# Optimization experiments

Hardware: AMD Instinct MI355X
Metric: run time of the kernel (lower is better)

## Reference

```python
import jax, jax.numpy as jnp
import numpy as np

N = 4096
IN_F = 256
OUT_F = 64
K = 4
ALPHA = 0.2  # LeakyReLU negative slope
NEG_INF = -9e15


def setup_inputs() -> dict:
    key = jax.random.key(0)
    k_h, k_w, k_a, k_e, k_m = jax.random.split(key, 5)
    h = jax.random.normal(k_h, (N, IN_F), dtype=jnp.float32)
    # xavier_uniform with gain=1.414
    def xavier(k, shape, gain=1.414):
        fan_in, fan_out = shape[0], shape[1]
        limit = gain * np.sqrt(6.0 / (fan_in + fan_out))
        return jax.random.uniform(k, shape, jnp.float32, -limit, limit)
    W = xavier(k_w, (IN_F, OUT_F))
    a = xavier(k_a, (2 * OUT_F, 1))
    vals = jax.random.uniform(k_e, (K, N, N), dtype=jnp.float32)
    mask = jax.random.uniform(k_m, (K, N, N), dtype=jnp.float32) < 0.05
    edge_attr = jnp.where(mask, vals, 0.0)
    return {"h": h, "edge_attr": edge_attr, "W": W, "a": a}


def reference(h, edge_attr, W, a):
    # h: [N, IN_F], edge_attr: [K, N, N], W: [IN_F, OUT_F], a: [2*OUT_F, 1]
    Wh = h @ W                                   # [N, OUT_F]
    Wh1 = Wh @ a[:OUT_F, :]                      # [N, 1]
    Wh2 = Wh @ a[OUT_F:, :]                      # [N, 1]
    e = jax.nn.leaky_relu(Wh1 + Wh2.T, negative_slope=ALPHA)  # [N, N]
    e = e[None, :, :] * edge_attr                # [K, N, N]
    e = jnp.where(edge_attr > 0, e, NEG_INF)
    att = jax.nn.softmax(e, axis=1)              # softmax over dim=1, as in torch
    # dropout is identity in eval mode
    # batched replacement for the per-channel python loop of matmuls
    hp = jnp.einsum('kij,jf->kif', att, Wh)      # [K, N, OUT_F]
    out = jnp.transpose(hp, (1, 0, 2)).reshape(N, K * OUT_F)  # concat dim=1
    return jax.nn.elu(out), att
```

## Files before the change

### kernel.cpp

```cpp
#include <hip/hip_runtime.h>

#define NN 4096
#define IN_F 256
#define OUT_F 64
#define K_CH 4
#define ALPHA 0.2f
#define JP 8
#define JCOLS 512
#define ROWS1 16
#define IC1 256

typedef __bf16 bf16;
typedef __attribute__((ext_vector_type(8))) __bf16 bf16x8;
typedef __attribute__((ext_vector_type(4))) float f32x4;

__global__ __launch_bounds__(256) void k0_wh(const float* __restrict__ h,
                                             const float* __restrict__ W,
                                             const float* __restrict__ a,
                                             float* __restrict__ Wh,
                                             float* __restrict__ Wh1,
                                             float* __restrict__ Wh2) {
    int tid = threadIdx.x;
    int wave = tid >> 6, lane = tid & 63;
    int i = blockIdx.x * 4 + wave;
    const float* hrow = h + (size_t)i * IN_F;
    float acc = 0.f;
    #pragma unroll 8
    for (int c = 0; c < IN_F; ++c)
        acc += hrow[c] * W[c * OUT_F + lane];
    Wh[(size_t)i * OUT_F + lane] = acc;
    float v1 = acc * a[lane];
    float v2 = acc * a[OUT_F + lane];
    #pragma unroll
    for (int o = 32; o > 0; o >>= 1) {
        v1 += __shfl_xor(v1, o, 64);
        v2 += __shfl_xor(v2, o, 64);
    }
    if (lane == 0) { Wh1[i] = v1; Wh2[i] = v2; }
}

__global__ __launch_bounds__(256) void k0_transpose(const float* __restrict__ Wh,
                                                    bf16* __restrict__ WhT) {
    __shared__ float lds[OUT_F * 65];
    int tid = threadIdx.x;
    int i0 = blockIdx.x * 64;
    int f = tid & 63;
    int r0 = tid >> 6;
    #pragma unroll
    for (int s = 0; s < 16; ++s) {
        int r = r0 * 16 + s;
        lds[f * 65 + r] = Wh[(size_t)(i0 + r) * OUT_F + f];
    }
    __syncthreads();
    int f2 = tid >> 2;
    int c0 = (tid & 3) * 16;
    #pragma unroll
    for (int s = 0; s < 16; ++s) {
        int c = c0 + s;
        WhT[(size_t)f2 * NN + i0 + c] = (bf16)lds[f2 * 65 + c];
    }
}

__global__ __launch_bounds__(256) void k1_colsum(const float* __restrict__ edge,
                                                 const float* __restrict__ Wh1,
                                                 const float* __restrict__ Wh2,
                                                 bf16* __restrict__ p_buf,
                                                 float* __restrict__ partial) {
    int tid = threadIdx.x;
    int kch = blockIdx.z;
    int j0 = blockIdx.y * 2048 + tid * 8;
    int ic = blockIdx.x;
    int ibase = ic * ROWS1;
    float w2[8];
    {
        f32x4 t0 = *(const f32x4*)&Wh2[j0];
        f32x4 t1 = *(const f32x4*)&Wh2[j0 + 4];
        #pragma unroll
        for (int c = 0; c < 4; ++c) { w2[c] = t0[c]; w2[c + 4] = t1[c]; }
    }
    float s[8] = {0.f, 0.f, 0.f, 0.f, 0.f, 0.f, 0.f, 0.f};
    const float* base = edge + ((size_t)kch * NN + ibase) * NN + j0;
    bf16* pbase = p_buf + ((size_t)kch * NN + ibase) * NN + j0;
    f32x4 r0[4], r1[4];
    #pragma unroll
    for (int t = 0; t < 4; ++t) {
        r0[t] = *(const f32x4*)(base + (size_t)t * NN);
        r1[t] = *(const f32x4*)(base + (size_t)t * NN + 4);
    }
    #pragma unroll 4
    for (int ii = 0; ii < ROWS1; ++ii) {
        int cur = ii & 3;
        f32x4 e0 = r0[cur], e1 = r1[cur];
        int ip = (ii + 4 < ROWS1) ? ii + 4 : ii;
        r0[cur] = *(const f32x4*)(base + (size_t)ip * NN);
        r1[cur] = *(const f32x4*)(base + (size_t)ip * NN + 4);
        float wh1 = Wh1[ibase + ii];
        bf16x8 pv;
        #pragma unroll
        for (int c = 0; c < 8; ++c) {
            float ef = c < 4 ? e0[c] : e1[c - 4];
            float xv = wh1 + w2[c];
            float lk = xv > 0.f ? xv : ALPHA * xv;
            float val = ef > 0.f ? __expf(lk * ef) : 0.f;
            bf16 vb = (bf16)val;
            pv[c] = vb;
            s[c] += (float)vb;
        }
        *(bf16x8*)(pbase + (size_t)ii * NN) = pv;
    }
    float* pr = partial + ((size_t)kch * IC1 + ic) * NN + j0;
    f32x4 o0, o1;
    #pragma unroll
    for (int c = 0; c < 4; ++c) { o0[c] = s[c]; o1[c] = s[c + 4]; }
    *(f32x4*)pr = o0;
    *(f32x4*)(pr + 4) = o1;
}

__global__ __launch_bounds__(256) void k1_reduce(const float* __restrict__ partial,
                                                 float* __restrict__ s_inv) {
    __shared__ float red[256];
    int tid = threadIdx.x;
    int kch = blockIdx.y;
    int jl = tid & 63, g = tid >> 6;
    int j = blockIdx.x * 64 + jl;
    const float* pb = partial + (size_t)kch * IC1 * NN;
    float s = 0.f;
    #pragma unroll 8
    for (int t = 0; t < IC1 / 4; ++t)
        s += pb[(size_t)(g * (IC1 / 4) + t) * NN + j];
    red[tid] = s;
    __syncthreads();
    if (tid < 64) {
        float tot = red[tid] + red[tid + 64] + red[tid + 128] + red[tid + 192];
        s_inv[kch * NN + j] = tot > 0.f ? 1.f / tot : 0.f;
    }
}

__global__ __launch_bounds__(256) void k2_fused(const bf16* __restrict__ p_buf,
                                                const float* __restrict__ s_inv,
                                                const bf16* __restrict__ WhT,
                                                float* __restrict__ att_out,
                                                float* __restrict__ hp) {
    __shared__ float lds_inv[JCOLS];
    int tid = threadIdx.x;
    int itile = blockIdx.x;
    int z = blockIdx.y;
    int kch = z >> 3, jp = z & 7;
    int jbase0 = jp * JCOLS;
    {
        int t2 = tid * 2;
        lds_inv[t2]     = s_inv[kch * NN + jbase0 + t2];
        lds_inv[t2 + 1] = s_inv[kch * NN + jbase0 + t2 + 1];
    }
    __syncthreads();
    int wave = tid >> 6, lane = tid & 63;
    int n16 = lane & 15, quad = lane >> 4;
    int i_row = itile * 64 + wave * 16 + n16;
    const size_t ebase = ((size_t)kch * NN + i_row) * NN + jbase0 + quad * 8;
    const bf16* pptr = p_buf + ebase;
    float* aptr = att_out + ebase;
    const bf16* wbase = WhT + (size_t)n16 * NN + jbase0 + quad * 8;
    f32x4 acc[4] = {};
    bf16x8 pf[4];
    #pragma unroll
    for (int t = 0; t < 4; ++t)
        pf[t] = *(const bf16x8*)(pptr + t * 32);
    #pragma unroll 4
    for (int s = 0; s < JCOLS / 32; ++s) {
        int cur = s & 3;
        bf16x8 pv = pf[cur];
        int sp = (s + 4 < JCOLS / 32) ? s + 4 : s;
        pf[cur] = *(const bf16x8*)(pptr + sp * 32);
        int jl = s * 32 + quad * 8;
        f32x4 iv0 = *(const f32x4*)&lds_inv[jl];
        f32x4 iv1 = *(const f32x4*)&lds_inv[jl + 4];
        bf16x8 afrag;
        f32x4 av0, av1;
        #pragma unroll
        for (int c = 0; c < 8; ++c) {
            float isc = c < 4 ? iv0[c] : iv1[c - 4];
            float attv = (float)pv[c] * isc;
            afrag[c] = (bf16)attv;
            if (c < 4) av0[c] = attv; else av1[c - 4] = attv;
        }
        __builtin_nontemporal_store(av0, (f32x4*)(aptr + s * 32));
        __builtin_nontemporal_store(av1, (f32x4*)(aptr + s * 32 + 4));
        #pragma unroll
        for (int ft = 0; ft < 4; ++ft) {
            bf16x8 bfrag = *(const bf16x8*)(wbase + (size_t)ft * 16 * NN + s * 32);
            acc[ft] = __builtin_amdgcn_mfma_f32_16x16x32_bf16(afrag, bfrag, acc[ft], 0, 0, 0);
        }
    }
    #pragma unroll
    for (int ft = 0; ft < 4; ++ft) {
        #pragma unroll
        for (int r = 0; r < 4; ++r) {
            int row_l = quad * 4 + r;
            int i_g = itile * 64 + wave * 16 + row_l;
            size_t idx = ((size_t)z * NN + i_g) * OUT_F + ft * 16 + n16;
            hp[idx] = acc[ft][r];
        }
    }
}

__global__ __launch_bounds__(256) void k3_combine(const float* __restrict__ hp,
                                                  float* __restrict__ out) {
    int g = blockIdx.x * 256 + threadIdx.x;
    int i = g >> 8;
    int rem = g & 255;
    int kch = rem >> 6;
    int f = rem & 63;
    float s = 0.f;
    #pragma unroll
    for (int z = 0; z < JP; ++z)
        s += hp[(((size_t)(kch * JP + z)) * NN + i) * OUT_F + f];
    out[g] = s > 0.f ? s : __expf(s) - 1.f;
}

extern "C" void kernel_launch(void* const* d_in, const int* in_sizes, int n_in,
                              void* d_out, int out_size, void* d_ws, size_t ws_size,
                              hipStream_t stream) {
    (void)out_size; (void)ws_size;
    const float *h = nullptr, *edge = nullptr, *W = nullptr, *a = nullptr;
    for (int i = 0; i < n_in; ++i) {
        int sz = in_sizes[i];
        if (sz == NN * IN_F)               h    = (const float*)d_in[i];
        else if (sz == K_CH * NN * NN)     edge = (const float*)d_in[i];
        else if (sz == IN_F * OUT_F)       W    = (const float*)d_in[i];
        else if (sz == 2 * OUT_F)          a    = (const float*)d_in[i];
    }

    char* ws = (char*)d_ws;
    size_t off = 0;
    float* Wh      = (float*)(ws + off); off += (size_t)NN * OUT_F * 4;
    float* Wh1     = (float*)(ws + off); off += NN * 4;
    float* Wh2     = (float*)(ws + off); off += NN * 4;
    float* s_inv   = (float*)(ws + off); off += (size_t)K_CH * NN * 4;
    bf16*  WhT     = (bf16*) (ws + off); off += (size_t)OUT_F * NN * 2;
    float* partial = (float*)(ws + off); off += (size_t)K_CH * IC1 * NN * 4;
    float* hp      = (float*)(ws + off); off += (size_t)K_CH * JP * NN * OUT_F * 4;
    bf16*  p_buf   = (bf16*) (ws + off); off += (size_t)K_CH * NN * NN * 2;

    float* out_h   = (float*)d_out;
    float* att_out = out_h + (size_t)NN * (K_CH * OUT_F);

    k0_wh<<<dim3(NN / 4), 256, 0, stream>>>(h, W, a, Wh, Wh1, Wh2);
    k0_transpose<<<dim3(NN / 64), 256, 0, stream>>>(Wh, WhT);
    k1_colsum<<<dim3(IC1, 2, K_CH), 256, 0, stream>>>(edge, Wh1, Wh2, p_buf, partial);
    k1_reduce<<<dim3(NN / 64, K_CH), 256, 0, stream>>>(partial, s_inv);
    k2_fused<<<dim3(64, K_CH * JP), 256, 0, stream>>>(p_buf, s_inv, WhT, att_out, hp);
    k3_combine<<<dim3((NN * K_CH * OUT_F) / 256), 256, 0, stream>>>(hp, out_h);
}
```

Before: 625.2 us.

## Stage WhT tile in padded LDS, halve column tiles, retile colsum kernel

```diff
diff --git a/kernel.cpp b/kernel.cpp
--- a/kernel.cpp
+++ b/kernel.cpp
@@ -5,13 +5,15 @@
 #define OUT_F 64
 #define K_CH 4
 #define ALPHA 0.2f
-#define JP 8
-#define JCOLS 512
-#define ROWS1 16
-#define IC1 256
+#define JP 16
+#define JCOLS 256
+#define ROWS1 32
+#define IC1 128
+#define BSTRIDE 264
 
 typedef __bf16 bf16;
 typedef __attribute__((ext_vector_type(8))) __bf16 bf16x8;
+typedef __attribute__((ext_vector_type(4))) __bf16 bf16x4;
 typedef __attribute__((ext_vector_type(4))) float f32x4;
 
 __global__ __launch_bounds__(256) void k0_wh(const float* __restrict__ h,
@@ -68,52 +70,37 @@
                                                  float* __restrict__ partial) {
     int tid = threadIdx.x;
     int kch = blockIdx.z;
-    int j0 = blockIdx.y * 2048 + tid * 8;
+    int j0 = blockIdx.y * 1024 + tid * 4;
     int ic = blockIdx.x;
     int ibase = ic * ROWS1;
-    float w2[8];
-    {
-        f32x4 t0 = *(const f32x4*)&Wh2[j0];
-        f32x4 t1 = *(const f32x4*)&Wh2[j0 + 4];
-        #pragma unroll
-        for (int c = 0; c < 4; ++c) { w2[c] = t0[c]; w2[c + 4] = t1[c]; }
-    }
-    float s[8] = {0.f, 0.f, 0.f, 0.f, 0.f, 0.f, 0.f, 0.f};
+    f32x4 w2 = *(const f32x4*)&Wh2[j0];
+    f32x4 s = {0.f, 0.f, 0.f, 0.f};
     const float* base = edge + ((size_t)kch * NN + ibase) * NN + j0;
     bf16* pbase = p_buf + ((size_t)kch * NN + ibase) * NN + j0;
-    f32x4 r0[4], r1[4];
-    #pragma unroll
-    for (int t = 0; t < 4; ++t) {
-        r0[t] = *(const f32x4*)(base + (size_t)t * NN);
-        r1[t] = *(const f32x4*)(base + (size_t)t * NN + 4);
-    }
-    #pragma unroll 4
+    f32x4 r[8];
+    #pragma unroll
+    for (int t = 0; t < 8; ++t)
+        r[t] = *(const f32x4*)(base + (size_t)t * NN);
+    #pragma unroll
     for (int ii = 0; ii < ROWS1; ++ii) {
-        int cur = ii & 3;
-        f32x4 e0 = r0[cur], e1 = r1[cur];
-        int ip = (ii + 4 < ROWS1) ? ii + 4 : ii;
-        r0[cur] = *(const f32x4*)(base + (size_t)ip * NN);
-        r1[cur] = *(const f32x4*)(base + (size_t)ip * NN + 4);
+        int cur = ii & 7;
+        f32x4 e = r[cur];
+        int ip = (ii + 8 < ROWS1) ? ii + 8 : ii;
+        r[cur] = *(const f32x4*)(base + (size_t)ip * NN);
         float wh1 = Wh1[ibase + ii];
-        bf16x8 pv;
-        #pragma unroll
-        for (int c = 0; c < 8; ++c) {
-            float ef = c < 4 ? e0[c] : e1[c - 4];
+        bf16x4 pv;
+        #pragma unroll
+        for (int c = 0; c < 4; ++c) {
             float xv = wh1 + w2[c];
             float lk = xv > 0.f ? xv : ALPHA * xv;
-            float val = ef > 0.f ? __expf(lk * ef) : 0.f;
+            float val = e[c] > 0.f ? __expf(lk * e[c]) : 0.f;
             bf16 vb = (bf16)val;
             pv[c] = vb;
             s[c] += (float)vb;
         }
-        *(bf16x8*)(pbase + (size_t)ii * NN) = pv;
-    }
-    float* pr = partial + ((size_t)kch * IC1 + ic) * NN + j0;
-    f32x4 o0, o1;
-    #pragma unroll
-    for (int c = 0; c < 4; ++c) { o0[c] = s[c]; o1[c] = s[c + 4]; }
-    *(f32x4*)pr = o0;
-    *(f32x4*)(pr + 4) = o1;
+        *(bf16x4*)(pbase + (size_t)ii * NN) = pv;
+    }
+    *(f32x4*)(partial + ((size_t)kch * IC1 + ic) * NN + j0) = s;
 }
 
 __global__ __launch_bounds__(256) void k1_reduce(const float* __restrict__ partial,
@@ -141,16 +128,21 @@
                                                 const bf16* __restrict__ WhT,
                                                 float* __restrict__ att_out,
                                                 float* __restrict__ hp) {
+    __shared__ bf16 ldsB[OUT_F * BSTRIDE];
     __shared__ float lds_inv[JCOLS];
     int tid = threadIdx.x;
     int itile = blockIdx.x;
     int z = blockIdx.y;
-    int kch = z >> 3, jp = z & 7;
+    int kch = z >> 4, jp = z & 15;
     int jbase0 = jp * JCOLS;
     {
-        int t2 = tid * 2;
-        lds_inv[t2]     = s_inv[kch * NN + jbase0 + t2];
-        lds_inv[t2 + 1] = s_inv[kch * NN + jbase0 + t2 + 1];
+        int f = tid >> 2, part = (tid & 3) * 64;
+        #pragma unroll
+        for (int u = 0; u < 8; ++u) {
+            bf16x8 v = *(const bf16x8*)(WhT + (size_t)f * NN + jbase0 + part + u * 8);
+            *(bf16x8*)&ldsB[f * BSTRIDE + part + u * 8] = v;
+        }
+        lds_inv[tid] = s_inv[kch * NN + jbase0 + tid];
     }
     __syncthreads();
     int wave = tid >> 6, lane = tid & 63;
@@ -159,13 +151,12 @@
     const size_t ebase = ((size_t)kch * NN + i_row) * NN + jbase0 + quad * 8;
     const bf16* pptr = p_buf + ebase;
     float* aptr = att_out + ebase;
-    const bf16* wbase = WhT + (size_t)n16 * NN + jbase0 + quad * 8;
     f32x4 acc[4] = {};
     bf16x8 pf[4];
     #pragma unroll
     for (int t = 0; t < 4; ++t)
         pf[t] = *(const bf16x8*)(pptr + t * 32);
-    #pragma unroll 4
+    #pragma unroll
     for (int s = 0; s < JCOLS / 32; ++s) {
         int cur = s & 3;
         bf16x8 pv = pf[cur];
@@ -183,11 +174,11 @@
             afrag[c] = (bf16)attv;
             if (c < 4) av0[c] = attv; else av1[c - 4] = attv;
         }
-        __builtin_nontemporal_store(av0, (f32x4*)(aptr + s * 32));
-        __builtin_nontemporal_store(av1, (f32x4*)(aptr + s * 32 + 4));
+        *(f32x4*)(aptr + s * 32) = av0;
+        *(f32x4*)(aptr + s * 32 + 4) = av1;
         #pragma unroll
         for (int ft = 0; ft < 4; ++ft) {
-            bf16x8 bfrag = *(const bf16x8*)(wbase + (size_t)ft * 16 * NN + s * 32);
+            bf16x8 bfrag = *(const bf16x8*)&ldsB[(ft * 16 + n16) * BSTRIDE + jl];
             acc[ft] = __builtin_amdgcn_mfma_f32_16x16x32_bf16(afrag, bfrag, acc[ft], 0, 0, 0);
         }
     }
@@ -246,7 +237,7 @@
 
     k0_wh<<<dim3(NN / 4), 256, 0, stream>>>(h, W, a, Wh, Wh1, Wh2);
     k0_transpose<<<dim3(NN / 64), 256, 0, stream>>>(Wh, WhT);
-    k1_colsum<<<dim3(IC1, 2, K_CH), 256, 0, stream>>>(edge, Wh1, Wh2, p_buf, partial);
+    k1_colsum<<<dim3(IC1, 4, K_CH), 256, 0, stream>>>(edge, Wh1, Wh2, p_buf, partial);
     k1_reduce<<<dim3(NN / 64, K_CH), 256, 0, stream>>>(partial, s_inv);
     k2_fused<<<dim3(64, K_CH * JP), 256, 0, stream>>>(p_buf, s_inv, WhT, att_out, hp);
     k3_combine<<<dim3((NN * K_CH * OUT_F) / 256), 256, 0, stream>>>(hp, out_h);
```

Measured after the change: 593.9 us. 1.05x faster.
